# Kernel optimization log

Measured on AMD Instinct MI355X. Metric: run time of the kernel, lower is better.

Reference implementation:

```python
import jax, jax.numpy as jnp
import numpy as np

N = 30000
E = 600000
IN = 64
HID = 128
EPS = 1e-5
HEADS_PER_LAYER = (4, 4, 1)


def _bn(x, g, b):
    # eval-mode BatchNorm: running_mean=0, running_var=1
    return x * (g / np.sqrt(1.0 + EPS)) + b


def _segment_softmax(e, dst, n):
    m = jax.ops.segment_max(e, dst, num_segments=n)
    ex = jnp.exp(e - m[dst])
    s = jax.ops.segment_sum(ex, dst, num_segments=n)
    return ex / (s[dst] + 1e-16)


def _gcn_conv(x, w, b, src, dst, norm, n):
    m = (x @ w)[src] * norm[:, None]            # [E+N, HID]
    return jax.ops.segment_sum(m, dst, num_segments=n) + b


def _gat_conv(x, w, a_src, a_dst, b, src, dst, n, heads):
    C = HID // heads
    xh = (x @ w).reshape(n, heads, C)
    asrc = (xh * a_src.reshape(heads, C)).sum(-1)   # [N, heads]
    adst = (xh * a_dst.reshape(heads, C)).sum(-1)
    e = jax.nn.leaky_relu(asrc[src] + adst[dst], 0.2)  # [E+N, heads]
    alpha = _segment_softmax(e, dst, n)
    out = jax.ops.segment_sum(xh[src] * alpha[:, :, None], dst, num_segments=n)
    return out.reshape(n, HID) + b


def _forward(x, gcn_in_w, gcn_in_b, gcn_res_w, gcn_res_b, gcn_w, gcn_b,
             gcn_bn_g, gcn_bn_b, gcn_c1w, gcn_c1b, gcn_c2w, gcn_c2b,
             gcn_c3w, gcn_c3b, gat_in_w, gat_in_b, gat_w, gat_asrc,
             gat_adst, gat_b, gat_bn_g, gat_bn_b, feat_imp, gat_c1w,
             gat_c1b, gat_cbn_g, gat_cbn_b, gat_c2w, gat_c2b, gat_c3w,
             gat_c3b, fin_w, fin_b, fin_bn_g, fin_bn_b, fin2_w, fin2_b,
             edge_index):
    n = x.shape[0]
    loop = jnp.arange(n, dtype=edge_index.dtype)
    src = jnp.concatenate([edge_index[0], loop])  # add self-loops
    dst = jnp.concatenate([edge_index[1], loop])
    # GCN symmetric normalization (with self-loops)
    deg = jax.ops.segment_sum(jnp.ones_like(dst, dtype=x.dtype), dst, num_segments=n)
    dis = jnp.where(deg > 0, jax.lax.rsqrt(jnp.maximum(deg, 1.0)), 0.0)
    norm = dis[src] * dis[dst]

    # ---- GCN branch (eval: dropout = identity, self-attn skipped since N>5000) ----
    xp = x @ gcn_in_w + gcn_in_b
    res = x @ gcn_res_w + gcn_res_b
    for i in range(3):
        xn = _gcn_conv(xp, gcn_w[i], gcn_b[i], src, dst, norm, n)
        xn = jax.nn.relu(_bn(xn, gcn_bn_g[i], gcn_bn_b[i]))
        if i % 2 == 1:
            xp = xn + res
            res = xp
        else:
            xp = xn
    h = jax.nn.relu(xp @ gcn_c1w + gcn_c1b)
    h = jax.nn.relu(h @ gcn_c2w + gcn_c2b)
    gcn_out = h @ gcn_c3w + gcn_c3b

    # ---- GAT branch ----
    xg = x @ gat_in_w + gat_in_b
    for i in range(3):
        xg = _gat_conv(xg, gat_w[i], gat_asrc[i], gat_adst[i], gat_b[i],
                       src, dst, n, HEADS_PER_LAYER[i])
        xg = jax.nn.elu(_bn(xg, gat_bn_g[i], gat_bn_b[i]))
    xg = xg * feat_imp
    h = jax.nn.relu(xg @ gat_c1w + gat_c1b)
    h = _bn(h, gat_cbn_g, gat_cbn_b)
    h = jax.nn.relu(h @ gat_c2w + gat_c2b)
    gat_out = h @ gat_c3w + gat_c3b

    # ---- fusion: N > 10000 -> weighted blend path ----
    fused = 0.6 * gcn_out + 0.4 * gat_out
    h = jax.nn.relu(fused @ fin_w + fin_b)
    h = _bn(h, fin_bn_g, fin_bn_b)
    return h @ fin2_w + fin2_b  # [N, 2]


def setup_inputs() -> dict:
    key = jax.random.key(0)
    ks = iter(jax.random.split(key, 64))

    def nrm(shape, scale=1.0):
        return jax.random.normal(next(ks), shape, dtype=jnp.float32) * scale

    s_in = 1.0 / np.sqrt(IN)
    s_h = 1.0 / np.sqrt(HID)
    inp = {}
    inp['x'] = nrm((N, IN))
    inp['edge_index'] = jax.random.randint(next(ks), (2, E), 0, N, dtype=jnp.int32)
    inp['gcn_in_w'] = nrm((IN, HID), s_in); inp['gcn_in_b'] = nrm((HID,), 0.01)
    inp['gcn_res_w'] = nrm((IN, HID), s_in); inp['gcn_res_b'] = nrm((HID,), 0.01)
    inp['gcn_w'] = nrm((3, HID, HID), s_h); inp['gcn_b'] = nrm((3, HID), 0.01)
    inp['gcn_bn_g'] = 1.0 + nrm((3, HID), 0.1); inp['gcn_bn_b'] = nrm((3, HID), 0.1)
    inp['gcn_c1w'] = nrm((HID, 64), s_h); inp['gcn_c1b'] = nrm((64,), 0.01)
    inp['gcn_c2w'] = nrm((64, 32), 0.125); inp['gcn_c2b'] = nrm((32,), 0.01)
    inp['gcn_c3w'] = nrm((32, HID), 0.18); inp['gcn_c3b'] = nrm((HID,), 0.01)
    inp['gat_in_w'] = nrm((IN, HID), s_in); inp['gat_in_b'] = nrm((HID,), 0.01)
    inp['gat_w'] = nrm((3, HID, HID), s_h)
    inp['gat_asrc'] = nrm((3, HID), s_h); inp['gat_adst'] = nrm((3, HID), s_h)
    inp['gat_b'] = nrm((3, HID), 0.01)
    inp['gat_bn_g'] = 1.0 + nrm((3, HID), 0.1); inp['gat_bn_b'] = nrm((3, HID), 0.1)
    inp['feat_imp'] = 1.0 + nrm((HID,), 0.1)
    inp['gat_c1w'] = nrm((HID, 64), s_h); inp['gat_c1b'] = nrm((64,), 0.01)
    inp['gat_cbn_g'] = 1.0 + nrm((64,), 0.1); inp['gat_cbn_b'] = nrm((64,), 0.1)
    inp['gat_c2w'] = nrm((64, 32), 0.125); inp['gat_c2b'] = nrm((32,), 0.01)
    inp['gat_c3w'] = nrm((32, HID), 0.18); inp['gat_c3b'] = nrm((HID,), 0.01)
    inp['fin_w'] = nrm((HID, 64), s_h); inp['fin_b'] = nrm((64,), 0.01)
    inp['fin_bn_g'] = 1.0 + nrm((64,), 0.1); inp['fin_bn_b'] = nrm((64,), 0.1)
    inp['fin2_w'] = nrm((64, 2), 0.125); inp['fin2_b'] = nrm((2,), 0.01)
    return inp


def reference(x, edge_index, gcn_in_w, gcn_in_b, gcn_res_w, gcn_res_b, gcn_w,
              gcn_b, gcn_bn_g, gcn_bn_b, gcn_c1w, gcn_c1b, gcn_c2w, gcn_c2b,
              gcn_c3w, gcn_c3b, gat_in_w, gat_in_b, gat_w, gat_asrc, gat_adst,
              gat_b, gat_bn_g, gat_bn_b, feat_imp, gat_c1w, gat_c1b, gat_cbn_g,
              gat_cbn_b, gat_c2w, gat_c2b, gat_c3w, gat_c3b, fin_w, fin_b,
              fin_bn_g, fin_bn_b, fin2_w, fin2_b):
    return _forward(x, gcn_in_w, gcn_in_b, gcn_res_w, gcn_res_b, gcn_w, gcn_b,
                    gcn_bn_g, gcn_bn_b, gcn_c1w, gcn_c1b, gcn_c2w, gcn_c2b,
                    gcn_c3w, gcn_c3b, gat_in_w, gat_in_b, gat_w, gat_asrc,
                    gat_adst, gat_b, gat_bn_g, gat_bn_b, feat_imp, gat_c1w,
                    gat_c1b, gat_cbn_g, gat_cbn_b, gat_c2w, gat_c2b, gat_c3w,
                    gat_c3b, fin_w, fin_b, fin_bn_g, fin_bn_b, fin2_w, fin2_b,
                    edge_index)
```

## Files before the change

kernel.cpp:

```cpp
#include <hip/hip_runtime.h>
#include <hip/hip_fp16.h>

#define RSQ_BN 0.9999950000374997f

typedef _Float16 f16x8 __attribute__((ext_vector_type(8)));
typedef float f32x4 __attribute__((ext_vector_type(4)));

__device__ __forceinline__ float leaky02(float x) { return x > 0.f ? x : 0.2f * x; }

__device__ __forceinline__ float4 ld4(const float* p) {
    return *reinterpret_cast<const float4*>(p);
}
__device__ __forceinline__ void st4(float* p, float4 v) {
    *reinterpret_cast<float4*>(p) = v;
}
__device__ __forceinline__ float4 h4f(uint2 u) {
    union { uint2 u; __half2 h[2]; } pk;
    pk.u = u;
    float2 lo = __half22float2(pk.h[0]);
    float2 hi = __half22float2(pk.h[1]);
    return make_float4(lo.x, lo.y, hi.x, hi.y);
}
__device__ __forceinline__ float4 f4z() { return make_float4(0.f, 0.f, 0.f, 0.f); }
__device__ __forceinline__ float4 f4bias(float4 v, float4 b) {
    return make_float4(v.x + b.x, v.y + b.y, v.z + b.z, v.w + b.w);
}
__device__ __forceinline__ float4 f4relu(float4 v) {
    return make_float4(fmaxf(v.x, 0.f), fmaxf(v.y, 0.f), fmaxf(v.z, 0.f), fmaxf(v.w, 0.f));
}
__device__ __forceinline__ float4 f4bn(float4 v, float4 g, float4 b) {
    return make_float4(v.x * g.x + b.x, v.y * g.y + b.y, v.z * g.z + b.z, v.w * g.w + b.w);
}
__device__ __forceinline__ float4 f4s(float4 v, float s) {
    return make_float4(v.x * s, v.y * s, v.z * s, v.w * s);
}


__global__ void zero_i32_k(int* __restrict__ p, int n) {
    int i = blockIdx.x * 256 + threadIdx.x;
    if (i < n) p[i] = 0;
}

__global__ void hist_k(const int* __restrict__ edst, int* __restrict__ cnt, int E, int EN) {
    int i = blockIdx.x * 256 + threadIdx.x;
    if (i >= EN) return;
    int d = (i < E) ? edst[i] : (i - E);
    atomicAdd(&cnt[d], 1);
}

__global__ __launch_bounds__(256)
void scanA_k(const int* __restrict__ cnt, int* __restrict__ rowptr,
             int* __restrict__ bsum, int n) {
    __shared__ int sh[256];
    int t = threadIdx.x;
    int i = blockIdx.x * 256 + t;
    int v = (i < n) ? cnt[i] : 0;
    sh[t] = v;
    __syncthreads();
#pragma unroll
    for (int off = 1; off < 256; off <<= 1) {
        int u = 0;
        if (t >= off) u = sh[t - off];
        __syncthreads();
        sh[t] += u;
        __syncthreads();
    }
    if (i < n) rowptr[i] = sh[t] - v;
    if (t == 255) bsum[blockIdx.x] = sh[255];
}

__global__ __launch_bounds__(256)
void scanB_k(int* __restrict__ bsum, int nb) {
    __shared__ int sh[256];
    int t = threadIdx.x;
    int v = (t < nb) ? bsum[t] : 0;
    sh[t] = v;
    __syncthreads();
#pragma unroll
    for (int off = 1; off < 256; off <<= 1) {
        int u = 0;
        if (t >= off) u = sh[t - off];
        __syncthreads();
        sh[t] += u;
        __syncthreads();
    }
    if (t < nb) bsum[t] = sh[t] - v;
}

__global__ __launch_bounds__(256)
void scanC_k(const int* __restrict__ cnt, const int* __restrict__ bsum,
             int* __restrict__ rowptr, int* __restrict__ cursor,
             float* __restrict__ dis, int n, int EN) {
    int i = blockIdx.x * 256 + threadIdx.x;
    if (i < n) {
        int r = rowptr[i] + bsum[blockIdx.x];
        rowptr[i] = r;
        cursor[i] = r;
        dis[i] = rsqrtf((float)cnt[i]);
    }
    if (i == 0) rowptr[n] = EN;
}

__global__ void scatter_k(const int* __restrict__ esrc, const int* __restrict__ edst,
                          int* __restrict__ cursor, int* __restrict__ colidx, int E, int EN) {
    int i = blockIdx.x * 256 + threadIdx.x;
    if (i >= EN) return;
    int s, d;
    if (i < E) { s = esrc[i]; d = edst[i]; }
    else       { s = i - E; d = s; }
    int pos = atomicAdd(&cursor[d], 1);
    colidx[pos] = s;
}


__global__ void wtx_all_k(const float* __restrict__ gcn_in_w, const float* __restrict__ gcn_res_w,
                          const float* __restrict__ gat_in_w,
                          const float* __restrict__ gcn_w, const float* __restrict__ gat_w,
                          const float* __restrict__ gcn_c1w, const float* __restrict__ gat_c1w,
                          const float* __restrict__ gcn_c3w, const float* __restrict__ gat_c3w,
                          const float* __restrict__ fin_w,
                          __half* __restrict__ WTin, __half* __restrict__ WTg,
                          __half* __restrict__ WTa, __half* __restrict__ WTc1,
                          __half* __restrict__ WTc3, __half* __restrict__ WTfin) {
    int idx = blockIdx.x * 256 + threadIdx.x;
    const float* src;
    __half* dst;
    int K, M, o;
    if (idx < 24576) {
        int mi = idx >> 13; o = idx & 8191;
        src = mi == 0 ? gcn_in_w : (mi == 1 ? gcn_res_w : gat_in_w);
        dst = WTin + mi * 8192; K = 64; M = 128;
    } else if (idx < 73728) {
        int r = idx - 24576; int mi = r >> 14; o = r & 16383;
        src = gcn_w + mi * 16384; dst = WTg + mi * 16384; K = 128; M = 128;
    } else if (idx < 122880) {
        int r = idx - 73728; int mi = r >> 14; o = r & 16383;
        src = gat_w + mi * 16384; dst = WTa + mi * 16384; K = 128; M = 128;
    } else if (idx < 139264) {
        int r = idx - 122880; int mi = r >> 13; o = r & 8191;
        src = mi ? gat_c1w : gcn_c1w; dst = WTc1 + mi * 8192; K = 128; M = 64;
    } else if (idx < 147456) {
        int r = idx - 139264; int mi = r >> 12; o = r & 4095;
        src = mi ? gat_c3w : gcn_c3w; dst = WTc3 + mi * 4096; K = 32; M = 128;
    } else if (idx < 155648) {
        o = idx - 147456; src = fin_w; dst = WTfin; K = 128; M = 64;
    } else return;
    int mcol = o / K, k = o - mcol * K;
    dst[o] = (__half)src[k * M + mcol];
}


#define FMA4R(A_, xv, w0, w1, w2, w3)                                  \
    A_.x += xv.x * w0.x + xv.y * w1.x + xv.z * w2.x + xv.w * w3.x;     \
    A_.y += xv.x * w0.y + xv.y * w1.y + xv.z * w2.y + xv.w * w3.y;     \
    A_.z += xv.x * w0.z + xv.y * w1.z + xv.z * w2.z + xv.w * w3.z;     \
    A_.w += xv.x * w0.w + xv.y * w1.w + xv.z * w2.w + xv.w * w3.w;

template <int K, int M>
__device__ __forceinline__ void gemm4(const float* __restrict__ Ws,
                                      const float* xa, const float* xb,
                                      const float* xc, const float* xd, int c,
                                      float4& A, float4& B, float4& C, float4& D) {
#pragma unroll 4
    for (int k = 0; k < K; k += 4) {
        float4 va = ld4(xa + k), vb = ld4(xb + k), vc = ld4(xc + k), vd = ld4(xd + k);
        const float* wp = Ws + k * M + c;
        float4 w0 = ld4(wp), w1 = ld4(wp + M), w2 = ld4(wp + 2 * M), w3 = ld4(wp + 3 * M);
        FMA4R(A, va, w0, w1, w2, w3)
        FMA4R(B, vb, w0, w1, w2, w3)
        FMA4R(C, vc, w0, w1, w2, w3)
        FMA4R(D, vd, w0, w1, w2, w3)
    }
}

template <int K, int M>
__global__ __launch_bounds__(256)
void tail2_k(const float* __restrict__ X0, const float* __restrict__ W0, const float* __restrict__ b0,
             float* __restrict__ Y0,
             const float* __restrict__ X1, const float* __restrict__ W1, const float* __restrict__ b1,
             float* __restrict__ Y1,
             int n, int gper, int do_relu) {
    constexpr int CG = M / 4, RPB = 256 / CG;
    bool s1 = blockIdx.x >= gper;
    int blk = s1 ? blockIdx.x - gper : blockIdx.x;
    const float* X = s1 ? X1 : X0;
    const float* W = s1 ? W1 : W0;
    const float* bi = s1 ? b1 : b0;
    float* Y = s1 ? Y1 : Y0;
    __shared__ float Ws[K * M];
    for (int i = threadIdx.x; i < K * M; i += 256) Ws[i] = W[i];
    __syncthreads();
    int cg = threadIdx.x % CG, r = threadIdx.x / CG, c = cg * 4;
    int ra = blk * (4 * RPB) + r, rb = ra + RPB, rc = ra + 2 * RPB, rd = ra + 3 * RPB;
    const float* xa = X + (size_t)(ra < n ? ra : 0) * K;
    const float* xb = X + (size_t)(rb < n ? rb : 0) * K;
    const float* xc = X + (size_t)(rc < n ? rc : 0) * K;
    const float* xd = X + (size_t)(rd < n ? rd : 0) * K;
    float4 A = f4z(), B = f4z(), C = f4z(), D = f4z();
    gemm4<K, M>(Ws, xa, xb, xc, xd, c, A, B, C, D);
    float4 bv = ld4(bi + c);
    A = f4bias(A, bv); B = f4bias(B, bv); C = f4bias(C, bv); D = f4bias(D, bv);
    if (do_relu) { A = f4relu(A); B = f4relu(B); C = f4relu(C); D = f4relu(D); }
    if (ra < n) st4(Y + (size_t)ra * M + c, A);
    if (rb < n) st4(Y + (size_t)rb * M + c, B);
    if (rc < n) st4(Y + (size_t)rc * M + c, C);
    if (rd < n) st4(Y + (size_t)rd * M + c, D);
}


__device__ __forceinline__ f16x8 mk_af(const float* xr, int kb) {
    float4 v0 = ld4(xr + kb), v1 = ld4(xr + kb + 4);
    f16x8 af;
    af[0] = (_Float16)v0.x; af[1] = (_Float16)v0.y;
    af[2] = (_Float16)v0.z; af[3] = (_Float16)v0.w;
    af[4] = (_Float16)v1.x; af[5] = (_Float16)v1.y;
    af[6] = (_Float16)v1.z; af[7] = (_Float16)v1.w;
    return af;
}

__global__ __launch_bounds__(256)
void mfma_lin3_k(const float* __restrict__ X, const __half* __restrict__ WTin,
                 const float* __restrict__ b0, float* __restrict__ Y0,
                 const float* __restrict__ b1, float* __restrict__ Y1,
                 const float* __restrict__ b2, float* __restrict__ Y2,
                 int n, int gper) {
    constexpr int K = 64, CT = 8;
    int set = blockIdx.x / gper, blk = blockIdx.x % gper;
    const __half* WT = WTin + (size_t)set * 8192;
    const float* bi = set == 0 ? b0 : (set == 1 ? b1 : b2);
    float* Y = set == 0 ? Y0 : (set == 1 ? Y1 : Y2);
    int wave = threadIdx.x >> 6, lane = threadIdx.x & 63;
    int m = lane & 15, quad = lane >> 4;
    int row0 = blk * 64 + wave * 16;
    int arow = min(row0 + m, n - 1);
    const float* xr = X + (size_t)arow * K;
    f32x4 acc[CT];
#pragma unroll
    for (int ct = 0; ct < CT; ++ct) acc[ct] = (f32x4){0.f, 0.f, 0.f, 0.f};
#pragma unroll
    for (int k32 = 0; k32 < K / 32; ++k32) {
        int kb = k32 * 32 + quad * 8;
        f16x8 af = mk_af(xr, kb);
#pragma unroll
        for (int ct = 0; ct < CT; ++ct) {
            f16x8 bf = *reinterpret_cast<const f16x8*>(WT + (size_t)(ct * 16 + m) * K + kb);
            acc[ct] = __builtin_amdgcn_mfma_f32_16x16x32_f16(af, bf, acc[ct], 0, 0, 0);
        }
    }
#pragma unroll
    for (int ct = 0; ct < CT; ++ct) {
        int col = ct * 16 + m;
        float cb = bi[col];
#pragma unroll
        for (int reg = 0; reg < 4; ++reg) {
            int row = row0 + quad * 4 + reg;
            if (row < n) Y[(size_t)row * 128 + col] = acc[ct][reg] + cb;
        }
    }
}

template <int K, int M>
__global__ __launch_bounds__(256)
void mfma_lin2_k(const float* __restrict__ X0, const __half* __restrict__ WT0,
                 const float* __restrict__ b0, const float* __restrict__ g0,
                 const float* __restrict__ bb0, float* __restrict__ Y0,
                 const float* __restrict__ X1, const __half* __restrict__ WT1,
                 const float* __restrict__ b1, const float* __restrict__ g1,
                 const float* __restrict__ bb1, float* __restrict__ Y1,
                 int n, int gper, int do_relu) {
    constexpr int CT = M / 16;
    bool s1 = blockIdx.x >= gper;
    int blk = s1 ? blockIdx.x - gper : blockIdx.x;
    const float* X = s1 ? X1 : X0;
    const __half* WT = s1 ? WT1 : WT0;
    const float* bi = s1 ? b1 : b0;
    const float* bg = s1 ? g1 : g0;
    const float* bb = s1 ? bb1 : bb0;
    float* Y = s1 ? Y1 : Y0;
    int wave = threadIdx.x >> 6, lane = threadIdx.x & 63;
    int m = lane & 15, quad = lane >> 4;
    int row0 = blk * 64 + wave * 16;
    int arow = min(row0 + m, n - 1);
    const float* xr = X + (size_t)arow * K;
    f32x4 acc[CT];
#pragma unroll
    for (int ct = 0; ct < CT; ++ct) acc[ct] = (f32x4){0.f, 0.f, 0.f, 0.f};
#pragma unroll
    for (int k32 = 0; k32 < K / 32; ++k32) {
        int kb = k32 * 32 + quad * 8;
        f16x8 af = mk_af(xr, kb);
#pragma unroll
        for (int ct = 0; ct < CT; ++ct) {
            f16x8 bf = *reinterpret_cast<const f16x8*>(WT + (size_t)(ct * 16 + m) * K + kb);
            acc[ct] = __builtin_amdgcn_mfma_f32_16x16x32_f16(af, bf, acc[ct], 0, 0, 0);
        }
    }
#pragma unroll
    for (int ct = 0; ct < CT; ++ct) {
        int col = ct * 16 + m;
        float cb = bi[col];
        float cg = bg ? bg[col] * RSQ_BN : 1.f;
        float cbb = bg ? bb[col] : 0.f;
#pragma unroll
        for (int reg = 0; reg < 4; ++reg) {
            int row = row0 + quad * 4 + reg;
            if (row < n) {
                float v = acc[ct][reg] + cb;
                if (do_relu) v = fmaxf(v, 0.f);
                if (bg) v = v * cg + cbb;
                Y[(size_t)row * M + col] = v;
            }
        }
    }
}

__global__ __launch_bounds__(256)
void mfma_linF_k(const float* __restrict__ XA, const float* __restrict__ XB,
                 const __half* __restrict__ WT, const float* __restrict__ bi,
                 const float* __restrict__ bg, const float* __restrict__ bb,
                 const float* __restrict__ w2, const float* __restrict__ b2,
                 float* __restrict__ out, int n) {
    constexpr int K = 128, M = 64, CT = 4;
    int wave = threadIdx.x >> 6, lane = threadIdx.x & 63;
    int m = lane & 15, quad = lane >> 4;
    int row0 = blockIdx.x * 64 + wave * 16;
    int arow = min(row0 + m, n - 1);
    const float* xra = XA + (size_t)arow * K;
    const float* xrb = XB + (size_t)arow * K;
    f32x4 acc[CT];
#pragma unroll
    for (int ct = 0; ct < CT; ++ct) acc[ct] = (f32x4){0.f, 0.f, 0.f, 0.f};
#pragma unroll
    for (int k32 = 0; k32 < K / 32; ++k32) {
        int kb = k32 * 32 + quad * 8;
        float4 a0 = ld4(xra + kb), a1 = ld4(xra + kb + 4);
        float4 u0 = ld4(xrb + kb), u1 = ld4(xrb + kb + 4);
        f16x8 af;
        af[0] = (_Float16)(0.6f * a0.x + 0.4f * u0.x);
        af[1] = (_Float16)(0.6f * a0.y + 0.4f * u0.y);
        af[2] = (_Float16)(0.6f * a0.z + 0.4f * u0.z);
        af[3] = (_Float16)(0.6f * a0.w + 0.4f * u0.w);
        af[4] = (_Float16)(0.6f * a1.x + 0.4f * u1.x);
        af[5] = (_Float16)(0.6f * a1.y + 0.4f * u1.y);
        af[6] = (_Float16)(0.6f * a1.z + 0.4f * u1.z);
        af[7] = (_Float16)(0.6f * a1.w + 0.4f * u1.w);
#pragma unroll
        for (int ct = 0; ct < CT; ++ct) {
            f16x8 bf = *reinterpret_cast<const f16x8*>(WT + (size_t)(ct * 16 + m) * K + kb);
            acc[ct] = __builtin_amdgcn_mfma_f32_16x16x32_f16(af, bf, acc[ct], 0, 0, 0);
        }
    }
    float p0[4] = {0.f, 0.f, 0.f, 0.f}, p1[4] = {0.f, 0.f, 0.f, 0.f};
#pragma unroll
    for (int ct = 0; ct < CT; ++ct) {
        int col = ct * 16 + m;
        float cb = bi[col];
        float cg = bg[col] * RSQ_BN;
        float cbb = bb[col];
        float w20 = w2[2 * col], w21 = w2[2 * col + 1];
#pragma unroll
        for (int reg = 0; reg < 4; ++reg) {
            float v = fmaxf(acc[ct][reg] + cb, 0.f) * cg + cbb;
            p0[reg] += v * w20;
            p1[reg] += v * w21;
        }
    }
    for (int off = 1; off < 16; off <<= 1) {
#pragma unroll
        for (int reg = 0; reg < 4; ++reg) {
            p0[reg] += __shfl_xor(p0[reg], off);
            p1[reg] += __shfl_xor(p1[reg], off);
        }
    }
    if (m == 0) {
#pragma unroll
        for (int reg = 0; reg < 4; ++reg) {
            int row = row0 + quad * 4 + reg;
            if (row < n) {
                out[row * 2] = p0[reg] + b2[0];
                out[row * 2 + 1] = p1[reg] + b2[1];
            }
        }
    }
}


__global__ __launch_bounds__(256)
void dual128_mfma_k(const float* __restrict__ Xg, const __half* __restrict__ WTg,
                    __half* __restrict__ Yg,
                    const float* __restrict__ Xa, const __half* __restrict__ WTa,
                    __half* __restrict__ Ya,
                    const float* __restrict__ dis,
                    const float* __restrict__ asrc, const float* __restrict__ adst,
                    float* __restrict__ avp, float* __restrict__ bvp,
                    int hh, int n, int gper) {
    bool gat = blockIdx.x >= gper;
    int blk = gat ? blockIdx.x - gper : blockIdx.x;
    const float* X = gat ? Xa : Xg;
    const __half* WT = gat ? WTa : WTg;
    __half* Y = gat ? Ya : Yg;
    int wave = threadIdx.x >> 6;
    int lane = threadIdx.x & 63;
    int m = lane & 15, quad = lane >> 4;
    int row0 = blk * 64 + wave * 16;
    int arow = min(row0 + m, n - 1);
    const float* xr = X + (size_t)arow * 128;
    f32x4 acc[8];
#pragma unroll
    for (int ct = 0; ct < 8; ++ct) acc[ct] = (f32x4){0.f, 0.f, 0.f, 0.f};
#pragma unroll
    for (int k32 = 0; k32 < 4; ++k32) {
        int kb = k32 * 32 + quad * 8;
        f16x8 af = mk_af(xr, kb);
#pragma unroll
        for (int ct = 0; ct < 8; ++ct) {
            f16x8 bf = *reinterpret_cast<const f16x8*>(WT + (size_t)(ct * 16 + m) * 128 + kb);
            acc[ct] = __builtin_amdgcn_mfma_f32_16x16x32_f16(af, bf, acc[ct], 0, 0, 0);
        }
    }
    if (!gat) {
#pragma unroll
        for (int reg = 0; reg < 4; ++reg) {
            int row = row0 + quad * 4 + reg;
            if (row < n) {
                float dv = dis[row];
#pragma unroll
                for (int ct = 0; ct < 8; ++ct)
                    Y[(size_t)row * 128 + ct * 16 + m] = (__half)(acc[ct][reg] * dv);
            }
        }
    } else {
        float cas[8], cad[8];
#pragma unroll
        for (int ct = 0; ct < 8; ++ct) {
            cas[ct] = asrc[ct * 16 + m];
            cad[ct] = adst[ct * 16 + m];
        }
        int ctph = 8 / hh;
#pragma unroll
        for (int reg = 0; reg < 4; ++reg) {
            int row = row0 + quad * 4 + reg;
            bool valid = row < n;
            if (valid) {
#pragma unroll
                for (int ct = 0; ct < 8; ++ct)
                    Y[(size_t)row * 128 + ct * 16 + m] = (__half)acc[ct][reg];
            }
            for (int h = 0; h < hh; ++h) {
                float sa = 0.f, sd = 0.f;
                for (int j = 0; j < ctph; ++j) {
                    int ct = h * ctph + j;
                    sa += acc[ct][reg] * cas[ct];
                    sd += acc[ct][reg] * cad[ct];
                }
                for (int off = 1; off < 16; off <<= 1) {
                    sa += __shfl_xor(sa, off);
                    sd += __shfl_xor(sd, off);
                }
                if (m == 0 && valid) {
                    avp[row * hh + h] = sa;
                    bvp[row * hh + h] = sd;
                }
            }
        }
    }
}


__global__ __launch_bounds__(256)
void fused_gather_k(const int* __restrict__ rowptr, const int* __restrict__ colidx,
                    const float* __restrict__ dis,
                    const __half* __restrict__ Tg, const float* __restrict__ gbias,
                    const float* __restrict__ gbng, const float* __restrict__ gbnb,
                    const float* __restrict__ res, float* __restrict__ Yg,
                    const __half* __restrict__ Ta, const float* __restrict__ avp,
                    const float* __restrict__ bvp, const float* __restrict__ abias,
                    const float* __restrict__ abng, const float* __restrict__ abnb,
                    const float* __restrict__ fimp, float* __restrict__ Ya,
                    int n, int hh, int log2C) {
    int idx = blockIdx.x * 256 + threadIdx.x;
    int i = idx >> 4;
    if (i >= n) return;
    int c = (idx & 15) * 8;
    int h = c >> log2C;
    float ad = bvp[i * hh + h];
    int p0 = rowptr[i], p1 = rowptr[i + 1];
    float4 glo = f4z(), ghi = f4z();
    float4 alo = f4z(), ahi = f4z();
    float m = -3.0e38f, s = 0.f;

#define GACC(qq)                                                                \
    {                                                                           \
        float4 t0 = h4f(make_uint2(qq.x, qq.y)), t1 = h4f(make_uint2(qq.z, qq.w)); \
        glo.x += t0.x; glo.y += t0.y; glo.z += t0.z; glo.w += t0.w;             \
        ghi.x += t1.x; ghi.y += t1.y; ghi.z += t1.z; ghi.w += t1.w;             \
    }
#define AACC(qq, ww)                                                            \
    {                                                                           \
        float4 t0 = h4f(make_uint2(qq.x, qq.y)), t1 = h4f(make_uint2(qq.z, qq.w)); \
        alo.x += t0.x * ww; alo.y += t0.y * ww; alo.z += t0.z * ww; alo.w += t0.w * ww; \
        ahi.x += t1.x * ww; ahi.y += t1.y * ww; ahi.z += t1.z * ww; ahi.w += t1.w * ww; \
    }

    int p = p0;
    int nfull = (p1 - p0) >> 2;
    int sx[4];
    if (nfull > 0) {
#pragma unroll
        for (int j = 0; j < 4; ++j) sx[j] = colidx[p + j];
    }
    for (int g = 0; g < nfull; ++g) {
        float e[4]; uint4 qg[4], qa[4];
#pragma unroll
        for (int j = 0; j < 4; ++j) e[j] = leaky02(avp[sx[j] * hh + h] + ad);
#pragma unroll
        for (int j = 0; j < 4; ++j)
            qg[j] = *reinterpret_cast<const uint4*>(Tg + (size_t)sx[j] * 128 + c);
#pragma unroll
        for (int j = 0; j < 4; ++j)
            qa[j] = *reinterpret_cast<const uint4*>(Ta + (size_t)sx[j] * 128 + c);
        int sn[4];
        int pn = p + 4;
        bool more = (g + 1) < nfull;
#pragma unroll
        for (int j = 0; j < 4; ++j) sn[j] = more ? colidx[pn + j] : 0;
#pragma unroll
        for (int j = 0; j < 4; ++j) GACC(qg[j])
        float mc = fmaxf(fmaxf(e[0], e[1]), fmaxf(e[2], e[3]));
        float mn = fmaxf(m, mc);
        float scale = expf(m - mn);
        alo = f4s(alo, scale);
        ahi = f4s(ahi, scale);
        float wsum = 0.f;
#pragma unroll
        for (int j = 0; j < 4; ++j) {
            float wj = expf(e[j] - mn);
            wsum += wj;
            AACC(qa[j], wj)
        }
        s = s * scale + wsum;
        m = mn;
        p = pn;
#pragma unroll
        for (int j = 0; j < 4; ++j) sx[j] = sn[j];
    }
    for (; p < p1; ++p) {
        int s0 = colidx[p];
        float e0 = leaky02(avp[s0 * hh + h] + ad);
        uint4 qg0 = *reinterpret_cast<const uint4*>(Tg + (size_t)s0 * 128 + c);
        uint4 qa0 = *reinterpret_cast<const uint4*>(Ta + (size_t)s0 * 128 + c);
        GACC(qg0)
        float mn = fmaxf(m, e0);
        float scale = expf(m - mn);
        float w0 = expf(e0 - mn);
        s = s * scale + w0;
        alo = f4s(alo, scale);
        ahi = f4s(ahi, scale);
        AACC(qa0, w0)
        m = mn;
    }

    {
        float di = dis[i];
        float4 b0 = ld4(gbias + c), b1 = ld4(gbias + c + 4);
        glo = make_float4(glo.x * di + b0.x, glo.y * di + b0.y, glo.z * di + b0.z, glo.w * di + b0.w);
        ghi = make_float4(ghi.x * di + b1.x, ghi.y * di + b1.y, ghi.z * di + b1.z, ghi.w * di + b1.w);
        float4 g0 = ld4(gbng + c), g1 = ld4(gbng + c + 4);
        g0 = f4s(g0, RSQ_BN); g1 = f4s(g1, RSQ_BN);
        float4 h0 = ld4(gbnb + c), h1 = ld4(gbnb + c + 4);
        glo = f4relu(f4bn(glo, g0, h0));
        ghi = f4relu(f4bn(ghi, g1, h1));
        if (res) {
            float4 r0 = ld4(res + (size_t)i * 128 + c), r1 = ld4(res + (size_t)i * 128 + c + 4);
            glo = f4bias(glo, r0); ghi = f4bias(ghi, r1);
        }
        st4(Yg + (size_t)i * 128 + c, glo);
        st4(Yg + (size_t)i * 128 + c + 4, ghi);
    }
    {
        float si = 1.f / (s + 1e-16f);
        float4 b0 = ld4(abias + c), b1 = ld4(abias + c + 4);
        alo = make_float4(alo.x * si + b0.x, alo.y * si + b0.y, alo.z * si + b0.z, alo.w * si + b0.w);
        ahi = make_float4(ahi.x * si + b1.x, ahi.y * si + b1.y, ahi.z * si + b1.z, ahi.w * si + b1.w);
        float4 g0 = ld4(abng + c), g1 = ld4(abng + c + 4);
        g0 = f4s(g0, RSQ_BN); g1 = f4s(g1, RSQ_BN);
        float4 h0 = ld4(abnb + c), h1 = ld4(abnb + c + 4);
        alo = f4bn(alo, g0, h0);
        ahi = f4bn(ahi, g1, h1);
        alo.x = alo.x > 0.f ? alo.x : expm1f(alo.x);
        alo.y = alo.y > 0.f ? alo.y : expm1f(alo.y);
        alo.z = alo.z > 0.f ? alo.z : expm1f(alo.z);
        alo.w = alo.w > 0.f ? alo.w : expm1f(alo.w);
        ahi.x = ahi.x > 0.f ? ahi.x : expm1f(ahi.x);
        ahi.y = ahi.y > 0.f ? ahi.y : expm1f(ahi.y);
        ahi.z = ahi.z > 0.f ? ahi.z : expm1f(ahi.z);
        ahi.w = ahi.w > 0.f ? ahi.w : expm1f(ahi.w);
        if (fimp) {
            float4 f0 = ld4(fimp + c), f1 = ld4(fimp + c + 4);
            alo = make_float4(alo.x * f0.x, alo.y * f0.y, alo.z * f0.z, alo.w * f0.w);
            ahi = make_float4(ahi.x * f1.x, ahi.y * f1.y, ahi.z * f1.z, ahi.w * f1.w);
        }
        st4(Ya + (size_t)i * 128 + c, alo);
        st4(Ya + (size_t)i * 128 + c + 4, ahi);
    }
#undef GACC
#undef AACC
}


static inline int cdiv(int a, int b) { return (a + b - 1) / b; }

extern "C" void kernel_launch(void* const* d_in, const int* in_sizes, int n_in,
                              void* d_out, int out_size, void* d_ws, size_t ws_size,
                              hipStream_t stream) {
    const float* x       = (const float*)d_in[0];
    const int*   ei      = (const int*)d_in[1];
    const float* gcn_in_w = (const float*)d_in[2];
    const float* gcn_in_b = (const float*)d_in[3];
    const float* gcn_res_w = (const float*)d_in[4];
    const float* gcn_res_b = (const float*)d_in[5];
    const float* gcn_w   = (const float*)d_in[6];
    const float* gcn_b   = (const float*)d_in[7];
    const float* gcn_bn_g = (const float*)d_in[8];
    const float* gcn_bn_b = (const float*)d_in[9];
    const float* gcn_c1w = (const float*)d_in[10];
    const float* gcn_c1b = (const float*)d_in[11];
    const float* gcn_c2w = (const float*)d_in[12];
    const float* gcn_c2b = (const float*)d_in[13];
    const float* gcn_c3w = (const float*)d_in[14];
    const float* gcn_c3b = (const float*)d_in[15];
    const float* gat_in_w = (const float*)d_in[16];
    const float* gat_in_b = (const float*)d_in[17];
    const float* gat_w   = (const float*)d_in[18];
    const float* gat_asrc = (const float*)d_in[19];
    const float* gat_adst = (const float*)d_in[20];
    const float* gat_b   = (const float*)d_in[21];
    const float* gat_bn_g = (const float*)d_in[22];
    const float* gat_bn_b = (const float*)d_in[23];
    const float* feat_imp = (const float*)d_in[24];
    const float* gat_c1w = (const float*)d_in[25];
    const float* gat_c1b = (const float*)d_in[26];
    const float* gat_cbn_g = (const float*)d_in[27];
    const float* gat_cbn_b = (const float*)d_in[28];
    const float* gat_c2w = (const float*)d_in[29];
    const float* gat_c2b = (const float*)d_in[30];
    const float* gat_c3w = (const float*)d_in[31];
    const float* gat_c3b = (const float*)d_in[32];
    const float* fin_w   = (const float*)d_in[33];
    const float* fin_b   = (const float*)d_in[34];
    const float* fin_bn_g = (const float*)d_in[35];
    const float* fin_bn_b = (const float*)d_in[36];
    const float* fin2_w  = (const float*)d_in[37];
    const float* fin2_b  = (const float*)d_in[38];

    const int N = in_sizes[0] / 64;
    const int E = in_sizes[1] / 2;
    const int EN = E + N;
    const int* esrc = ei;
    const int* edst = ei + E;

    char* wp = (char*)d_ws;
    auto alloc = [&](size_t bytes) -> void* {
        void* p = (void*)wp;
        wp += (bytes + 255) & ~(size_t)255;
        return p;
    };
    int* cnt    = (int*)alloc((size_t)N * 4);
    int* rowptr = (int*)alloc((size_t)(N + 1) * 4);
    int* cursor = (int*)alloc((size_t)N * 4);
    int* bsum   = (int*)alloc((size_t)256 * 4);
    int* colidx = (int*)alloc((size_t)EN * 4);
    float* dis  = (float*)alloc((size_t)N * 4);
    float* A    = (float*)alloc((size_t)N * 128 * 4);
    float* B    = (float*)alloc((size_t)N * 128 * 4);
    float* G    = (float*)alloc((size_t)N * 128 * 4);
    float* H    = (float*)alloc((size_t)N * 128 * 4);
    float* R    = (float*)alloc((size_t)N * 128 * 4);
    __half* Th1 = (__half*)alloc((size_t)N * 128 * 2);
    __half* Th2 = (__half*)alloc((size_t)N * 128 * 2);
    float* h2g  = (float*)alloc((size_t)N * 32 * 4);
    float* h2a  = (float*)alloc((size_t)N * 32 * 4);
    float* avv  = (float*)alloc((size_t)N * 4 * 4);
    float* bvv  = (float*)alloc((size_t)N * 4 * 4);
    __half* WTin = (__half*)alloc((size_t)3 * 8192 * 2);
    __half* WTg  = (__half*)alloc((size_t)3 * 16384 * 2);
    __half* WTa  = (__half*)alloc((size_t)3 * 16384 * 2);
    __half* WTc1 = (__half*)alloc((size_t)2 * 8192 * 2);
    __half* WTc3 = (__half*)alloc((size_t)2 * 4096 * 2);
    __half* WTfin = (__half*)alloc((size_t)8192 * 2);
    float* h1g = (float*)Th1;
    float* h1a = (float*)Th2;

    const int nScanB = cdiv(N, 256);
    zero_i32_k<<<cdiv(N, 256), 256, 0, stream>>>(cnt, N);
    hist_k<<<cdiv(EN, 256), 256, 0, stream>>>(edst, cnt, E, EN);
    scanA_k<<<nScanB, 256, 0, stream>>>(cnt, rowptr, bsum, N);
    scanB_k<<<1, 256, 0, stream>>>(bsum, nScanB);
    scanC_k<<<nScanB, 256, 0, stream>>>(cnt, bsum, rowptr, cursor, dis, N, EN);
    scatter_k<<<cdiv(EN, 256), 256, 0, stream>>>(esrc, edst, cursor, colidx, E, EN);
    wtx_all_k<<<608, 256, 0, stream>>>(gcn_in_w, gcn_res_w, gat_in_w, gcn_w, gat_w,
                                       gcn_c1w, gat_c1w, gcn_c3w, gat_c3w, fin_w,
                                       WTin, WTg, WTa, WTc1, WTc3, WTfin);

    const int g64r  = cdiv(N, 64);
    const int g128r = cdiv(N, 128);
    const int gG    = cdiv(N, 16);

    mfma_lin3_k<<<3 * g64r, 256, 0, stream>>>(x, WTin, gcn_in_b, A, gcn_res_b, R,
                                              gat_in_b, G, N, g64r);

    const int heads_arr[3] = {4, 4, 1};
    float* gcur = A; float* gnxt = B;
    float* acur = G; float* anxt = H;
    for (int i = 0; i < 3; ++i) {
        int hh = heads_arr[i];
        int log2C = (hh == 4) ? 5 : 7;
        dual128_mfma_k<<<2 * g64r, 256, 0, stream>>>(gcur, WTg + (size_t)i * 16384, Th1,
                                                     acur, WTa + (size_t)i * 16384, Th2, dis,
                                                     gat_asrc + i * 128, gat_adst + i * 128,
                                                     avv, bvv, hh, N, g64r);
        fused_gather_k<<<gG, 256, 0, stream>>>(rowptr, colidx, dis,
                                               Th1, gcn_b + i * 128, gcn_bn_g + i * 128,
                                               gcn_bn_b + i * 128, (i == 1) ? R : nullptr, gnxt,
                                               Th2, avv, bvv, gat_b + i * 128,
                                               gat_bn_g + i * 128, gat_bn_b + i * 128,
                                               (i == 2) ? feat_imp : nullptr, anxt,
                                               N, hh, log2C);
        float* t = gcur; gcur = gnxt; gnxt = t;
        t = acur; acur = anxt; anxt = t;
    }

    mfma_lin2_k<128, 64><<<2 * g64r, 256, 0, stream>>>(
        gcur, WTc1, gcn_c1b, nullptr, nullptr, h1g,
        acur, WTc1 + 8192, gat_c1b, gat_cbn_g, gat_cbn_b, h1a, N, g64r, 1);
    tail2_k<64, 32><<<2 * g128r, 256, 0, stream>>>(
        h1g, gcn_c2w, gcn_c2b, h2g,
        h1a, gat_c2w, gat_c2b, h2a, N, g128r, 1);
    mfma_lin2_k<32, 128><<<2 * g64r, 256, 0, stream>>>(
        h2g, WTc3, gcn_c3b, nullptr, nullptr, A,
        h2a, WTc3 + 4096, gat_c3b, nullptr, nullptr, G, N, g64r, 0);

    mfma_linF_k<<<g64r, 256, 0, stream>>>(A, G, WTfin, fin_b, fin_bn_g, fin_bn_b,
                                          fin2_w, fin2_b, (float*)d_out, N);
}
```

Measured before the change: 510.3 us.

## Fuse MLP tail into one MFMA kernel and streamline the GAT gather loop

Replaces the four tail kernels (c1 linear, fp32 c2 linear, c3 linear, final head) with a single kernel that keeps the intermediates in shared memory as fp16 and uses MFMA for every stage, including c2, whose weights are now transposed to fp16. The gather loop is also reworked: the next group's attention logits are prefetched, expf becomes __expf, and accumulation uses scalar arrays. This removes the global-memory round trips and launches between tail stages, at the cost of extra fp16 rounding and fast-exp precision. The zero kernel is replaced by hipMemsetAsync.

```diff
diff --git a/kernel.cpp b/kernel.cpp
--- a/kernel.cpp
+++ b/kernel.cpp
@@ -6,6 +6,8 @@
 typedef _Float16 f16x8 __attribute__((ext_vector_type(8)));
 typedef float f32x4 __attribute__((ext_vector_type(4)));
 
+union H8u { uint4 u4; __half h[8]; };
+
 __device__ __forceinline__ float leaky02(float x) { return x > 0.f ? x : 0.2f * x; }
 
 __device__ __forceinline__ float4 ld4(const float* p) {
@@ -14,32 +16,16 @@
 __device__ __forceinline__ void st4(float* p, float4 v) {
     *reinterpret_cast<float4*>(p) = v;
 }
-__device__ __forceinline__ float4 h4f(uint2 u) {
-    union { uint2 u; __half2 h[2]; } pk;
-    pk.u = u;
-    float2 lo = __half22float2(pk.h[0]);
-    float2 hi = __half22float2(pk.h[1]);
-    return make_float4(lo.x, lo.y, hi.x, hi.y);
-}
-__device__ __forceinline__ float4 f4z() { return make_float4(0.f, 0.f, 0.f, 0.f); }
-__device__ __forceinline__ float4 f4bias(float4 v, float4 b) {
-    return make_float4(v.x + b.x, v.y + b.y, v.z + b.z, v.w + b.w);
-}
-__device__ __forceinline__ float4 f4relu(float4 v) {
-    return make_float4(fmaxf(v.x, 0.f), fmaxf(v.y, 0.f), fmaxf(v.z, 0.f), fmaxf(v.w, 0.f));
-}
-__device__ __forceinline__ float4 f4bn(float4 v, float4 g, float4 b) {
-    return make_float4(v.x * g.x + b.x, v.y * g.y + b.y, v.z * g.z + b.z, v.w * g.w + b.w);
-}
-__device__ __forceinline__ float4 f4s(float4 v, float s) {
-    return make_float4(v.x * s, v.y * s, v.z * s, v.w * s);
-}
-
-
-__global__ void zero_i32_k(int* __restrict__ p, int n) {
-    int i = blockIdx.x * 256 + threadIdx.x;
-    if (i < n) p[i] = 0;
-}
+__device__ __forceinline__ void ld8(float* d, const float* p) {
+    float4 u = ld4(p), v = ld4(p + 4);
+    d[0] = u.x; d[1] = u.y; d[2] = u.z; d[3] = u.w;
+    d[4] = v.x; d[5] = v.y; d[6] = v.z; d[7] = v.w;
+}
+__device__ __forceinline__ void st8(float* p, const float* v) {
+    st4(p, make_float4(v[0], v[1], v[2], v[3]));
+    st4(p + 4, make_float4(v[4], v[5], v[6], v[7]));
+}
+
 
 __global__ void hist_k(const int* __restrict__ edst, int* __restrict__ cnt, int E, int EN) {
     int i = blockIdx.x * 256 + threadIdx.x;
@@ -119,9 +105,11 @@
                           const float* __restrict__ gcn_c1w, const float* __restrict__ gat_c1w,
                           const float* __restrict__ gcn_c3w, const float* __restrict__ gat_c3w,
                           const float* __restrict__ fin_w,
+                          const float* __restrict__ gcn_c2w, const float* __restrict__ gat_c2w,
                           __half* __restrict__ WTin, __half* __restrict__ WTg,
                           __half* __restrict__ WTa, __half* __restrict__ WTc1,
-                          __half* __restrict__ WTc3, __half* __restrict__ WTfin) {
+                          __half* __restrict__ WTc3, __half* __restrict__ WTfin,
+                          __half* __restrict__ WTc2) {
     int idx = blockIdx.x * 256 + threadIdx.x;
     const float* src;
     __half* dst;
@@ -144,67 +132,12 @@
         src = mi ? gat_c3w : gcn_c3w; dst = WTc3 + mi * 4096; K = 32; M = 128;
     } else if (idx < 155648) {
         o = idx - 147456; src = fin_w; dst = WTfin; K = 128; M = 64;
+    } else if (idx < 159744) {
+        int r = idx - 155648; int mi = r >> 11; o = r & 2047;
+        src = mi ? gat_c2w : gcn_c2w; dst = WTc2 + mi * 2048; K = 64; M = 32;
     } else return;
     int mcol = o / K, k = o - mcol * K;
     dst[o] = (__half)src[k * M + mcol];
-}
-
-
-#define FMA4R(A_, xv, w0, w1, w2, w3)                                  \
-    A_.x += xv.x * w0.x + xv.y * w1.x + xv.z * w2.x + xv.w * w3.x;     \
-    A_.y += xv.x * w0.y + xv.y * w1.y + xv.z * w2.y + xv.w * w3.y;     \
-    A_.z += xv.x * w0.z + xv.y * w1.z + xv.z * w2.z + xv.w * w3.z;     \
-    A_.w += xv.x * w0.w + xv.y * w1.w + xv.z * w2.w + xv.w * w3.w;
-
-template <int K, int M>
-__device__ __forceinline__ void gemm4(const float* __restrict__ Ws,
-                                      const float* xa, const float* xb,
-                                      const float* xc, const float* xd, int c,
-                                      float4& A, float4& B, float4& C, float4& D) {
-#pragma unroll 4
-    for (int k = 0; k < K; k += 4) {
-        float4 va = ld4(xa + k), vb = ld4(xb + k), vc = ld4(xc + k), vd = ld4(xd + k);
-        const float* wp = Ws + k * M + c;
-        float4 w0 = ld4(wp), w1 = ld4(wp + M), w2 = ld4(wp + 2 * M), w3 = ld4(wp + 3 * M);
-        FMA4R(A, va, w0, w1, w2, w3)
-        FMA4R(B, vb, w0, w1, w2, w3)
-        FMA4R(C, vc, w0, w1, w2, w3)
-        FMA4R(D, vd, w0, w1, w2, w3)
-    }
-}
-
-template <int K, int M>
-__global__ __launch_bounds__(256)
-void tail2_k(const float* __restrict__ X0, const float* __restrict__ W0, const float* __restrict__ b0,
-             float* __restrict__ Y0,
-             const float* __restrict__ X1, const float* __restrict__ W1, const float* __restrict__ b1,
-             float* __restrict__ Y1,
-             int n, int gper, int do_relu) {
-    constexpr int CG = M / 4, RPB = 256 / CG;
-    bool s1 = blockIdx.x >= gper;
-    int blk = s1 ? blockIdx.x - gper : blockIdx.x;
-    const float* X = s1 ? X1 : X0;
-    const float* W = s1 ? W1 : W0;
-    const float* bi = s1 ? b1 : b0;
-    float* Y = s1 ? Y1 : Y0;
-    __shared__ float Ws[K * M];
-    for (int i = threadIdx.x; i < K * M; i += 256) Ws[i] = W[i];
-    __syncthreads();
-    int cg = threadIdx.x % CG, r = threadIdx.x / CG, c = cg * 4;
-    int ra = blk * (4 * RPB) + r, rb = ra + RPB, rc = ra + 2 * RPB, rd = ra + 3 * RPB;
-    const float* xa = X + (size_t)(ra < n ? ra : 0) * K;
-    const float* xb = X + (size_t)(rb < n ? rb : 0) * K;
-    const float* xc = X + (size_t)(rc < n ? rc : 0) * K;
-    const float* xd = X + (size_t)(rd < n ? rd : 0) * K;
-    float4 A = f4z(), B = f4z(), C = f4z(), D = f4z();
-    gemm4<K, M>(Ws, xa, xb, xc, xd, c, A, B, C, D);
-    float4 bv = ld4(bi + c);
-    A = f4bias(A, bv); B = f4bias(B, bv); C = f4bias(C, bv); D = f4bias(D, bv);
-    if (do_relu) { A = f4relu(A); B = f4relu(B); C = f4relu(C); D = f4relu(D); }
-    if (ra < n) st4(Y + (size_t)ra * M + c, A);
-    if (rb < n) st4(Y + (size_t)rb * M + c, B);
-    if (rc < n) st4(Y + (size_t)rc * M + c, C);
-    if (rd < n) st4(Y + (size_t)rd * M + c, D);
 }
 
 
@@ -255,131 +188,6 @@
         for (int reg = 0; reg < 4; ++reg) {
             int row = row0 + quad * 4 + reg;
             if (row < n) Y[(size_t)row * 128 + col] = acc[ct][reg] + cb;
-        }
-    }
-}
-
-template <int K, int M>
-__global__ __launch_bounds__(256)
-void mfma_lin2_k(const float* __restrict__ X0, const __half* __restrict__ WT0,
-                 const float* __restrict__ b0, const float* __restrict__ g0,
-                 const float* __restrict__ bb0, float* __restrict__ Y0,
-                 const float* __restrict__ X1, const __half* __restrict__ WT1,
-                 const float* __restrict__ b1, const float* __restrict__ g1,
-                 const float* __restrict__ bb1, float* __restrict__ Y1,
-                 int n, int gper, int do_relu) {
-    constexpr int CT = M / 16;
-    bool s1 = blockIdx.x >= gper;
-    int blk = s1 ? blockIdx.x - gper : blockIdx.x;
-    const float* X = s1 ? X1 : X0;
-    const __half* WT = s1 ? WT1 : WT0;
-    const float* bi = s1 ? b1 : b0;
-    const float* bg = s1 ? g1 : g0;
-    const float* bb = s1 ? bb1 : bb0;
-    float* Y = s1 ? Y1 : Y0;
-    int wave = threadIdx.x >> 6, lane = threadIdx.x & 63;
-    int m = lane & 15, quad = lane >> 4;
-    int row0 = blk * 64 + wave * 16;
-    int arow = min(row0 + m, n - 1);
-    const float* xr = X + (size_t)arow * K;
-    f32x4 acc[CT];
-#pragma unroll
-    for (int ct = 0; ct < CT; ++ct) acc[ct] = (f32x4){0.f, 0.f, 0.f, 0.f};
-#pragma unroll
-    for (int k32 = 0; k32 < K / 32; ++k32) {
-        int kb = k32 * 32 + quad * 8;
-        f16x8 af = mk_af(xr, kb);
-#pragma unroll
-        for (int ct = 0; ct < CT; ++ct) {
-            f16x8 bf = *reinterpret_cast<const f16x8*>(WT + (size_t)(ct * 16 + m) * K + kb);
-            acc[ct] = __builtin_amdgcn_mfma_f32_16x16x32_f16(af, bf, acc[ct], 0, 0, 0);
-        }
-    }
-#pragma unroll
-    for (int ct = 0; ct < CT; ++ct) {
-        int col = ct * 16 + m;
-        float cb = bi[col];
-        float cg = bg ? bg[col] * RSQ_BN : 1.f;
-        float cbb = bg ? bb[col] : 0.f;
-#pragma unroll
-        for (int reg = 0; reg < 4; ++reg) {
-            int row = row0 + quad * 4 + reg;
-            if (row < n) {
-                float v = acc[ct][reg] + cb;
-                if (do_relu) v = fmaxf(v, 0.f);
-                if (bg) v = v * cg + cbb;
-                Y[(size_t)row * M + col] = v;
-            }
-        }
-    }
-}
-
-__global__ __launch_bounds__(256)
-void mfma_linF_k(const float* __restrict__ XA, const float* __restrict__ XB,
-                 const __half* __restrict__ WT, const float* __restrict__ bi,
-                 const float* __restrict__ bg, const float* __restrict__ bb,
-                 const float* __restrict__ w2, const float* __restrict__ b2,
-                 float* __restrict__ out, int n) {
-    constexpr int K = 128, M = 64, CT = 4;
-    int wave = threadIdx.x >> 6, lane = threadIdx.x & 63;
-    int m = lane & 15, quad = lane >> 4;
-    int row0 = blockIdx.x * 64 + wave * 16;
-    int arow = min(row0 + m, n - 1);
-    const float* xra = XA + (size_t)arow * K;
-    const float* xrb = XB + (size_t)arow * K;
-    f32x4 acc[CT];
-#pragma unroll
-    for (int ct = 0; ct < CT; ++ct) acc[ct] = (f32x4){0.f, 0.f, 0.f, 0.f};
-#pragma unroll
-    for (int k32 = 0; k32 < K / 32; ++k32) {
-        int kb = k32 * 32 + quad * 8;
-        float4 a0 = ld4(xra + kb), a1 = ld4(xra + kb + 4);
-        float4 u0 = ld4(xrb + kb), u1 = ld4(xrb + kb + 4);
-        f16x8 af;
-        af[0] = (_Float16)(0.6f * a0.x + 0.4f * u0.x);
-        af[1] = (_Float16)(0.6f * a0.y + 0.4f * u0.y);
-        af[2] = (_Float16)(0.6f * a0.z + 0.4f * u0.z);
-        af[3] = (_Float16)(0.6f * a0.w + 0.4f * u0.w);
-        af[4] = (_Float16)(0.6f * a1.x + 0.4f * u1.x);
-        af[5] = (_Float16)(0.6f * a1.y + 0.4f * u1.y);
-        af[6] = (_Float16)(0.6f * a1.z + 0.4f * u1.z);
-        af[7] = (_Float16)(0.6f * a1.w + 0.4f * u1.w);
-#pragma unroll
-        for (int ct = 0; ct < CT; ++ct) {
-            f16x8 bf = *reinterpret_cast<const f16x8*>(WT + (size_t)(ct * 16 + m) * K + kb);
-            acc[ct] = __builtin_amdgcn_mfma_f32_16x16x32_f16(af, bf, acc[ct], 0, 0, 0);
-        }
-    }
-    float p0[4] = {0.f, 0.f, 0.f, 0.f}, p1[4] = {0.f, 0.f, 0.f, 0.f};
-#pragma unroll
-    for (int ct = 0; ct < CT; ++ct) {
-        int col = ct * 16 + m;
-        float cb = bi[col];
-        float cg = bg[col] * RSQ_BN;
-        float cbb = bb[col];
-        float w20 = w2[2 * col], w21 = w2[2 * col + 1];
-#pragma unroll
-        for (int reg = 0; reg < 4; ++reg) {
-            float v = fmaxf(acc[ct][reg] + cb, 0.f) * cg + cbb;
-            p0[reg] += v * w20;
-            p1[reg] += v * w21;
-        }
-    }
-    for (int off = 1; off < 16; off <<= 1) {
-#pragma unroll
-        for (int reg = 0; reg < 4; ++reg) {
-            p0[reg] += __shfl_xor(p0[reg], off);
-            p1[reg] += __shfl_xor(p1[reg], off);
-        }
-    }
-    if (m == 0) {
-#pragma unroll
-        for (int reg = 0; reg < 4; ++reg) {
-            int row = row0 + quad * 4 + reg;
-            if (row < n) {
-                out[row * 2] = p0[reg] + b2[0];
-                out[row * 2 + 1] = p1[reg] + b2[1];
-            }
         }
     }
 }
@@ -485,126 +293,284 @@
     int h = c >> log2C;
     float ad = bvp[i * hh + h];
     int p0 = rowptr[i], p1 = rowptr[i + 1];
-    float4 glo = f4z(), ghi = f4z();
-    float4 alo = f4z(), ahi = f4z();
+    float g[8], a[8];
+#pragma unroll
+    for (int t = 0; t < 8; ++t) { g[t] = 0.f; a[t] = 0.f; }
     float m = -3.0e38f, s = 0.f;
-
-#define GACC(qq)                                                                \
-    {                                                                           \
-        float4 t0 = h4f(make_uint2(qq.x, qq.y)), t1 = h4f(make_uint2(qq.z, qq.w)); \
-        glo.x += t0.x; glo.y += t0.y; glo.z += t0.z; glo.w += t0.w;             \
-        ghi.x += t1.x; ghi.y += t1.y; ghi.z += t1.z; ghi.w += t1.w;             \
-    }
-#define AACC(qq, ww)                                                            \
-    {                                                                           \
-        float4 t0 = h4f(make_uint2(qq.x, qq.y)), t1 = h4f(make_uint2(qq.z, qq.w)); \
-        alo.x += t0.x * ww; alo.y += t0.y * ww; alo.z += t0.z * ww; alo.w += t0.w * ww; \
-        ahi.x += t1.x * ww; ahi.y += t1.y * ww; ahi.z += t1.z * ww; ahi.w += t1.w * ww; \
-    }
 
     int p = p0;
     int nfull = (p1 - p0) >> 2;
-    int sx[4];
+    int sx[4]; float av[4];
     if (nfull > 0) {
 #pragma unroll
         for (int j = 0; j < 4; ++j) sx[j] = colidx[p + j];
-    }
-    for (int g = 0; g < nfull; ++g) {
-        float e[4]; uint4 qg[4], qa[4];
-#pragma unroll
-        for (int j = 0; j < 4; ++j) e[j] = leaky02(avp[sx[j] * hh + h] + ad);
+#pragma unroll
+        for (int j = 0; j < 4; ++j) av[j] = avp[sx[j] * hh + h];
+    }
+    for (int gi = 0; gi < nfull; ++gi) {
+        uint4 qg[4], qa[4];
 #pragma unroll
         for (int j = 0; j < 4; ++j)
             qg[j] = *reinterpret_cast<const uint4*>(Tg + (size_t)sx[j] * 128 + c);
 #pragma unroll
         for (int j = 0; j < 4; ++j)
             qa[j] = *reinterpret_cast<const uint4*>(Ta + (size_t)sx[j] * 128 + c);
-        int sn[4];
         int pn = p + 4;
-        bool more = (g + 1) < nfull;
+        bool more = (gi + 1) < nfull;
+        int sn[4]; float avn[4];
 #pragma unroll
         for (int j = 0; j < 4; ++j) sn[j] = more ? colidx[pn + j] : 0;
 #pragma unroll
-        for (int j = 0; j < 4; ++j) GACC(qg[j])
-        float mc = fmaxf(fmaxf(e[0], e[1]), fmaxf(e[2], e[3]));
+        for (int j = 0; j < 4; ++j) avn[j] = avp[sn[j] * hh + h];
+        float e0 = leaky02(av[0] + ad), e1 = leaky02(av[1] + ad);
+        float e2 = leaky02(av[2] + ad), e3 = leaky02(av[3] + ad);
+        float mc = fmaxf(fmaxf(e0, e1), fmaxf(e2, e3));
         float mn = fmaxf(m, mc);
-        float scale = expf(m - mn);
-        alo = f4s(alo, scale);
-        ahi = f4s(ahi, scale);
-        float wsum = 0.f;
-#pragma unroll
-        for (int j = 0; j < 4; ++j) {
-            float wj = expf(e[j] - mn);
-            wsum += wj;
-            AACC(qa[j], wj)
-        }
-        s = s * scale + wsum;
+        float scale = __expf(m - mn);
+        float w0 = __expf(e0 - mn), w1 = __expf(e1 - mn);
+        float w2 = __expf(e2 - mn), w3 = __expf(e3 - mn);
+        s = s * scale + (w0 + w1 + w2 + w3);
         m = mn;
+        {
+            H8u k0, k1, k2, k3;
+            k0.u4 = qg[0]; k1.u4 = qg[1]; k2.u4 = qg[2]; k3.u4 = qg[3];
+#pragma unroll
+            for (int t = 0; t < 8; ++t)
+                g[t] += __half2float(k0.h[t]) + __half2float(k1.h[t])
+                      + __half2float(k2.h[t]) + __half2float(k3.h[t]);
+        }
+        {
+            H8u k0, k1, k2, k3;
+            k0.u4 = qa[0]; k1.u4 = qa[1]; k2.u4 = qa[2]; k3.u4 = qa[3];
+#pragma unroll
+            for (int t = 0; t < 8; ++t) {
+                float v = a[t] * scale;
+                v = fmaf(__half2float(k0.h[t]), w0, v);
+                v = fmaf(__half2float(k1.h[t]), w1, v);
+                v = fmaf(__half2float(k2.h[t]), w2, v);
+                v = fmaf(__half2float(k3.h[t]), w3, v);
+                a[t] = v;
+            }
+        }
         p = pn;
 #pragma unroll
-        for (int j = 0; j < 4; ++j) sx[j] = sn[j];
+        for (int j = 0; j < 4; ++j) { sx[j] = sn[j]; av[j] = avn[j]; }
     }
     for (; p < p1; ++p) {
         int s0 = colidx[p];
         float e0 = leaky02(avp[s0 * hh + h] + ad);
         uint4 qg0 = *reinterpret_cast<const uint4*>(Tg + (size_t)s0 * 128 + c);
         uint4 qa0 = *reinterpret_cast<const uint4*>(Ta + (size_t)s0 * 128 + c);
-        GACC(qg0)
         float mn = fmaxf(m, e0);
-        float scale = expf(m - mn);
-        float w0 = expf(e0 - mn);
+        float scale = __expf(m - mn);
+        float w0 = __expf(e0 - mn);
         s = s * scale + w0;
-        alo = f4s(alo, scale);
-        ahi = f4s(ahi, scale);
-        AACC(qa0, w0)
         m = mn;
+        H8u kg, ka; kg.u4 = qg0; ka.u4 = qa0;
+#pragma unroll
+        for (int t = 0; t < 8; ++t) {
+            g[t] += __half2float(kg.h[t]);
+            a[t] = fmaf(__half2float(ka.h[t]), w0, a[t] * scale);
+        }
     }
 
     {
         float di = dis[i];
-        float4 b0 = ld4(gbias + c), b1 = ld4(gbias + c + 4);
-        glo = make_float4(glo.x * di + b0.x, glo.y * di + b0.y, glo.z * di + b0.z, glo.w * di + b0.w);
-        ghi = make_float4(ghi.x * di + b1.x, ghi.y * di + b1.y, ghi.z * di + b1.z, ghi.w * di + b1.w);
-        float4 g0 = ld4(gbng + c), g1 = ld4(gbng + c + 4);
-        g0 = f4s(g0, RSQ_BN); g1 = f4s(g1, RSQ_BN);
-        float4 h0 = ld4(gbnb + c), h1 = ld4(gbnb + c + 4);
-        glo = f4relu(f4bn(glo, g0, h0));
-        ghi = f4relu(f4bn(ghi, g1, h1));
+        float bb[8], gg[8], nb[8];
+        ld8(bb, gbias + c); ld8(gg, gbng + c); ld8(nb, gbnb + c);
+        float o[8];
+#pragma unroll
+        for (int t = 0; t < 8; ++t) {
+            float v = g[t] * di + bb[t];
+            o[t] = fmaxf(v * (gg[t] * RSQ_BN) + nb[t], 0.f);
+        }
         if (res) {
-            float4 r0 = ld4(res + (size_t)i * 128 + c), r1 = ld4(res + (size_t)i * 128 + c + 4);
-            glo = f4bias(glo, r0); ghi = f4bias(ghi, r1);
-        }
-        st4(Yg + (size_t)i * 128 + c, glo);
-        st4(Yg + (size_t)i * 128 + c + 4, ghi);
+            float rr[8]; ld8(rr, res + (size_t)i * 128 + c);
+#pragma unroll
+            for (int t = 0; t < 8; ++t) o[t] += rr[t];
+        }
+        st8(Yg + (size_t)i * 128 + c, o);
     }
     {
         float si = 1.f / (s + 1e-16f);
-        float4 b0 = ld4(abias + c), b1 = ld4(abias + c + 4);
-        alo = make_float4(alo.x * si + b0.x, alo.y * si + b0.y, alo.z * si + b0.z, alo.w * si + b0.w);
-        ahi = make_float4(ahi.x * si + b1.x, ahi.y * si + b1.y, ahi.z * si + b1.z, ahi.w * si + b1.w);
-        float4 g0 = ld4(abng + c), g1 = ld4(abng + c + 4);
-        g0 = f4s(g0, RSQ_BN); g1 = f4s(g1, RSQ_BN);
-        float4 h0 = ld4(abnb + c), h1 = ld4(abnb + c + 4);
-        alo = f4bn(alo, g0, h0);
-        ahi = f4bn(ahi, g1, h1);
-        alo.x = alo.x > 0.f ? alo.x : expm1f(alo.x);
-        alo.y = alo.y > 0.f ? alo.y : expm1f(alo.y);
-        alo.z = alo.z > 0.f ? alo.z : expm1f(alo.z);
-        alo.w = alo.w > 0.f ? alo.w : expm1f(alo.w);
-        ahi.x = ahi.x > 0.f ? ahi.x : expm1f(ahi.x);
-        ahi.y = ahi.y > 0.f ? ahi.y : expm1f(ahi.y);
-        ahi.z = ahi.z > 0.f ? ahi.z : expm1f(ahi.z);
-        ahi.w = ahi.w > 0.f ? ahi.w : expm1f(ahi.w);
+        float bb[8], gg[8], nb[8];
+        ld8(bb, abias + c); ld8(gg, abng + c); ld8(nb, abnb + c);
+        float o[8];
+#pragma unroll
+        for (int t = 0; t < 8; ++t) {
+            float v = a[t] * si + bb[t];
+            v = v * (gg[t] * RSQ_BN) + nb[t];
+            o[t] = v > 0.f ? v : expm1f(v);
+        }
         if (fimp) {
-            float4 f0 = ld4(fimp + c), f1 = ld4(fimp + c + 4);
-            alo = make_float4(alo.x * f0.x, alo.y * f0.y, alo.z * f0.z, alo.w * f0.w);
-            ahi = make_float4(ahi.x * f1.x, ahi.y * f1.y, ahi.z * f1.z, ahi.w * f1.w);
-        }
-        st4(Ya + (size_t)i * 128 + c, alo);
-        st4(Ya + (size_t)i * 128 + c + 4, ahi);
-    }
-#undef GACC
-#undef AACC
+            float ff[8]; ld8(ff, fimp + c);
+#pragma unroll
+            for (int t = 0; t < 8; ++t) o[t] *= ff[t];
+        }
+        st8(Ya + (size_t)i * 128 + c, o);
+    }
+}
+
+
+__global__ __launch_bounds__(256)
+void fused_tail_k(const float* __restrict__ Xg, const float* __restrict__ Xa,
+                  const __half* __restrict__ WTc1,
+                  const float* __restrict__ c1bg, const float* __restrict__ c1ba,
+                  const float* __restrict__ cbng, const float* __restrict__ cbnb,
+                  const __half* __restrict__ WTc2,
+                  const float* __restrict__ c2bg, const float* __restrict__ c2ba,
+                  const __half* __restrict__ WTc3,
+                  const float* __restrict__ c3bg, const float* __restrict__ c3ba,
+                  const __half* __restrict__ WTfin, const float* __restrict__ finb,
+                  const float* __restrict__ fbng, const float* __restrict__ fbnb,
+                  const float* __restrict__ w2, const float* __restrict__ b2,
+                  float* __restrict__ out, int n) {
+    __shared__ alignas(16) __half h1s[2][64][88];
+    __shared__ alignas(16) __half h2s[2][64][56];
+    __shared__ alignas(16) __half Fs[64][152];
+    int wave = threadIdx.x >> 6, lane = threadIdx.x & 63;
+    int m = lane & 15, quad = lane >> 4;
+    int row0 = blockIdx.x * 64 + wave * 16;
+    int lr0 = wave * 16;
+    int arow = min(row0 + m, n - 1);
+
+#pragma unroll
+    for (int br = 0; br < 2; ++br) {
+        const float* xr = (br ? Xa : Xg) + (size_t)arow * 128;
+        const __half* WT = WTc1 + br * 8192;
+        f32x4 acc[4];
+#pragma unroll
+        for (int ct = 0; ct < 4; ++ct) acc[ct] = (f32x4){0.f, 0.f, 0.f, 0.f};
+#pragma unroll
+        for (int k32 = 0; k32 < 4; ++k32) {
+            int kb = k32 * 32 + quad * 8;
+            f16x8 af = mk_af(xr, kb);
+#pragma unroll
+            for (int ct = 0; ct < 4; ++ct) {
+                f16x8 bf = *reinterpret_cast<const f16x8*>(WT + (ct * 16 + m) * 128 + kb);
+                acc[ct] = __builtin_amdgcn_mfma_f32_16x16x32_f16(af, bf, acc[ct], 0, 0, 0);
+            }
+        }
+        const float* bi = br ? c1ba : c1bg;
+#pragma unroll
+        for (int ct = 0; ct < 4; ++ct) {
+            int col = ct * 16 + m;
+            float cb = bi[col];
+            float cg = br ? cbng[col] * RSQ_BN : 1.f;
+            float cbb = br ? cbnb[col] : 0.f;
+#pragma unroll
+            for (int reg = 0; reg < 4; ++reg) {
+                float v = fmaxf(acc[ct][reg] + cb, 0.f) * cg + cbb;
+                h1s[br][lr0 + quad * 4 + reg][col] = (__half)v;
+            }
+        }
+    }
+    __syncthreads();
+#pragma unroll
+    for (int br = 0; br < 2; ++br) {
+        f32x4 acc[2];
+        acc[0] = (f32x4){0.f, 0.f, 0.f, 0.f};
+        acc[1] = (f32x4){0.f, 0.f, 0.f, 0.f};
+        const __half* WT = WTc2 + br * 2048;
+#pragma unroll
+        for (int k32 = 0; k32 < 2; ++k32) {
+            int kb = k32 * 32 + quad * 8;
+            f16x8 af = *reinterpret_cast<const f16x8*>(&h1s[br][lr0 + m][kb]);
+#pragma unroll
+            for (int ct = 0; ct < 2; ++ct) {
+                f16x8 bf = *reinterpret_cast<const f16x8*>(WT + (ct * 16 + m) * 64 + kb);
+                acc[ct] = __builtin_amdgcn_mfma_f32_16x16x32_f16(af, bf, acc[ct], 0, 0, 0);
+            }
+        }
+        const float* bi = br ? c2ba : c2bg;
+#pragma unroll
+        for (int ct = 0; ct < 2; ++ct) {
+            int col = ct * 16 + m;
+            float cb = bi[col];
+#pragma unroll
+            for (int reg = 0; reg < 4; ++reg) {
+                float v = fmaxf(acc[ct][reg] + cb, 0.f);
+                h2s[br][lr0 + quad * 4 + reg][col] = (__half)v;
+            }
+        }
+    }
+    __syncthreads();
+    {
+        f32x4 ag[8], aa[8];
+#pragma unroll
+        for (int ct = 0; ct < 8; ++ct) {
+            ag[ct] = (f32x4){0.f, 0.f, 0.f, 0.f};
+            aa[ct] = (f32x4){0.f, 0.f, 0.f, 0.f};
+        }
+        int kb = quad * 8;
+        f16x8 afg = *reinterpret_cast<const f16x8*>(&h2s[0][lr0 + m][kb]);
+        f16x8 afa = *reinterpret_cast<const f16x8*>(&h2s[1][lr0 + m][kb]);
+#pragma unroll
+        for (int ct = 0; ct < 8; ++ct) {
+            f16x8 bfg = *reinterpret_cast<const f16x8*>(WTc3 + (ct * 16 + m) * 32 + kb);
+            f16x8 bfa = *reinterpret_cast<const f16x8*>(WTc3 + 4096 + (ct * 16 + m) * 32 + kb);
+            ag[ct] = __builtin_amdgcn_mfma_f32_16x16x32_f16(afg, bfg, ag[ct], 0, 0, 0);
+            aa[ct] = __builtin_amdgcn_mfma_f32_16x16x32_f16(afa, bfa, aa[ct], 0, 0, 0);
+        }
+#pragma unroll
+        for (int ct = 0; ct < 8; ++ct) {
+            int col = ct * 16 + m;
+            float cb = 0.6f * c3bg[col] + 0.4f * c3ba[col];
+#pragma unroll
+            for (int reg = 0; reg < 4; ++reg) {
+                float v = 0.6f * ag[ct][reg] + 0.4f * aa[ct][reg] + cb;
+                Fs[lr0 + quad * 4 + reg][col] = (__half)v;
+            }
+        }
+    }
+    __syncthreads();
+    {
+        f32x4 acc[4];
+#pragma unroll
+        for (int ct = 0; ct < 4; ++ct) acc[ct] = (f32x4){0.f, 0.f, 0.f, 0.f};
+#pragma unroll
+        for (int k32 = 0; k32 < 4; ++k32) {
+            int kb = k32 * 32 + quad * 8;
+            f16x8 af = *reinterpret_cast<const f16x8*>(&Fs[lr0 + m][kb]);
+#pragma unroll
+            for (int ct = 0; ct < 4; ++ct) {
+                f16x8 bf = *reinterpret_cast<const f16x8*>(WTfin + (ct * 16 + m) * 128 + kb);
+                acc[ct] = __builtin_amdgcn_mfma_f32_16x16x32_f16(af, bf, acc[ct], 0, 0, 0);
+            }
+        }
+        float p0[4] = {0.f, 0.f, 0.f, 0.f}, p1[4] = {0.f, 0.f, 0.f, 0.f};
+#pragma unroll
+        for (int ct = 0; ct < 4; ++ct) {
+            int col = ct * 16 + m;
+            float cb = finb[col];
+            float cg = fbng[col] * RSQ_BN;
+            float cbb = fbnb[col];
+            float w20 = w2[2 * col], w21 = w2[2 * col + 1];
+#pragma unroll
+            for (int reg = 0; reg < 4; ++reg) {
+                float v = fmaxf(acc[ct][reg] + cb, 0.f) * cg + cbb;
+                p0[reg] += v * w20;
+                p1[reg] += v * w21;
+            }
+        }
+        for (int off = 1; off < 16; off <<= 1) {
+#pragma unroll
+            for (int reg = 0; reg < 4; ++reg) {
+                p0[reg] += __shfl_xor(p0[reg], off);
+                p1[reg] += __shfl_xor(p1[reg], off);
+            }
+        }
+        if (m == 0) {
+#pragma unroll
+            for (int reg = 0; reg < 4; ++reg) {
+                int row = row0 + quad * 4 + reg;
+                if (row < n) {
+                    out[row * 2] = p0[reg] + b2[0];
+                    out[row * 2 + 1] = p1[reg] + b2[1];
+                }
+            }
+        }
+    }
 }
 
 
@@ -678,8 +644,6 @@
     float* R    = (float*)alloc((size_t)N * 128 * 4);
     __half* Th1 = (__half*)alloc((size_t)N * 128 * 2);
     __half* Th2 = (__half*)alloc((size_t)N * 128 * 2);
-    float* h2g  = (float*)alloc((size_t)N * 32 * 4);
-    float* h2a  = (float*)alloc((size_t)N * 32 * 4);
     float* avv  = (float*)alloc((size_t)N * 4 * 4);
     float* bvv  = (float*)alloc((size_t)N * 4 * 4);
     __half* WTin = (__half*)alloc((size_t)3 * 8192 * 2);
@@ -688,23 +652,22 @@
     __half* WTc1 = (__half*)alloc((size_t)2 * 8192 * 2);
     __half* WTc3 = (__half*)alloc((size_t)2 * 4096 * 2);
     __half* WTfin = (__half*)alloc((size_t)8192 * 2);
-    float* h1g = (float*)Th1;
-    float* h1a = (float*)Th2;
+    __half* WTc2 = (__half*)alloc((size_t)2 * 2048 * 2);
 
     const int nScanB = cdiv(N, 256);
-    zero_i32_k<<<cdiv(N, 256), 256, 0, stream>>>(cnt, N);
+    hipMemsetAsync(cnt, 0, (size_t)N * 4, stream);
     hist_k<<<cdiv(EN, 256), 256, 0, stream>>>(edst, cnt, E, EN);
     scanA_k<<<nScanB, 256, 0, stream>>>(cnt, rowptr, bsum, N);
     scanB_k<<<1, 256, 0, stream>>>(bsum, nScanB);
     scanC_k<<<nScanB, 256, 0, stream>>>(cnt, bsum, rowptr, cursor, dis, N, EN);
     scatter_k<<<cdiv(EN, 256), 256, 0, stream>>>(esrc, edst, cursor, colidx, E, EN);
-    wtx_all_k<<<608, 256, 0, stream>>>(gcn_in_w, gcn_res_w, gat_in_w, gcn_w, gat_w,
+    wtx_all_k<<<624, 256, 0, stream>>>(gcn_in_w, gcn_res_w, gat_in_w, gcn_w, gat_w,
                                        gcn_c1w, gat_c1w, gcn_c3w, gat_c3w, fin_w,
-                                       WTin, WTg, WTa, WTc1, WTc3, WTfin);
-
-    const int g64r  = cdiv(N, 64);
-    const int g128r = cdiv(N, 128);
-    const int gG    = cdiv(N, 16);
+                                       gcn_c2w, gat_c2w,
+                                       WTin, WTg, WTa, WTc1, WTc3, WTfin, WTc2);
+
+    const int g64r = cdiv(N, 64);
+    const int gG   = cdiv(N, 16);
 
     mfma_lin3_k<<<3 * g64r, 256, 0, stream>>>(x, WTin, gcn_in_b, A, gcn_res_b, R,
                                               gat_in_b, G, N, g64r);
@@ -730,16 +693,10 @@
         t = acur; acur = anxt; anxt = t;
     }
 
-    mfma_lin2_k<128, 64><<<2 * g64r, 256, 0, stream>>>(
-        gcur, WTc1, gcn_c1b, nullptr, nullptr, h1g,
-        acur, WTc1 + 8192, gat_c1b, gat_cbn_g, gat_cbn_b, h1a, N, g64r, 1);
-    tail2_k<64, 32><<<2 * g128r, 256, 0, stream>>>(
-        h1g, gcn_c2w, gcn_c2b, h2g,
-        h1a, gat_c2w, gat_c2b, h2a, N, g128r, 1);
-    mfma_lin2_k<32, 128><<<2 * g64r, 256, 0, stream>>>(
-        h2g, WTc3, gcn_c3b, nullptr, nullptr, A,
-        h2a, WTc3 + 4096, gat_c3b, nullptr, nullptr, G, N, g64r, 0);
-
-    mfma_linF_k<<<g64r, 256, 0, stream>>>(A, G, WTfin, fin_b, fin_bn_g, fin_bn_b,
-                                          fin2_w, fin2_b, (float*)d_out, N);
-}
+    fused_tail_k<<<g64r, 256, 0, stream>>>(gcur, acur,
+                                           WTc1, gcn_c1b, gat_c1b, gat_cbn_g, gat_cbn_b,
+                                           WTc2, gcn_c2b, gat_c2b,
+                                           WTc3, gcn_c3b, gat_c3b,
+                                           WTfin, fin_b, fin_bn_g, fin_bn_b,
+                                           fin2_w, fin2_b, (float*)d_out, N);
+}
```

Result: faster. 481.0 us (-5.7%).
